# Performance work log

Hardware: AMD Instinct MI355X
Metric: run time of the kernel (lower is better)

Reference implementation:

```python
import jax, jax.numpy as jnp
import numpy as np

B, N, T = 1024, 16, 256


def setup_inputs() -> dict:
    key = jax.random.key(0)
    k1, k2, k3 = jax.random.split(key, 3)
    prediction = jax.random.normal(k1, (B, N, T), dtype=jnp.float32)
    target = jax.random.normal(k2, (B, N, T), dtype=jnp.float32)
    # cov must be symmetric positive definite per (batch, time): A A^T + I
    A = 0.3 * jax.random.normal(k3, (B, T, N, N), dtype=jnp.float32)
    cov_bt = A @ jnp.swapaxes(A, -1, -2) + jnp.eye(N, dtype=jnp.float32)  # [B,T,N,N]
    cov = jnp.transpose(cov_bt, (0, 2, 3, 1))  # [B,N,N,T] as the module expects
    return {"prediction": prediction, "target": target, "cov": cov}


def reference(prediction, target, cov):
    # prediction/target: [B,N,T], cov: [B,N,N,T]
    diff = jnp.transpose(prediction - target, (0, 2, 1))        # [B,T,N]
    cov_bt = jnp.transpose(cov, (0, 3, 1, 2))                   # [B,T,N,N]
    inv_sigma = jnp.linalg.inv(cov_bt)                          # [B,T,N,N]
    # quadratic form diff^T Sigma^{-1} diff per (batch, time)
    quad = jnp.einsum('btn,btnm,btm->bt', diff, inv_sigma, diff)  # [B,T]
    logdet = jnp.log(jnp.linalg.det(cov_bt))                      # [B,T]
    # original: sum_t [mean_b quad_t + mean_b logdet_t] / T == mean over (b,t)
    return jnp.mean(quad + logdet)
```

## Files before the change

### kernel.cpp

```cpp
#include <hip/hip_runtime.h>


#define B_ 1024
#define N_ 16
#define T_ 256
#define TRI (N_ * (N_ + 1) / 2)

__global__ __launch_bounds__(256) void gll_main(
    const float* __restrict__ pred,
    const float* __restrict__ targ,
    const float* __restrict__ cov,
    float* __restrict__ partial)
{
    const int b = blockIdx.x;
    const int t = threadIdx.x;

    float d[N_];
    const size_t pbase = (size_t)b * N_ * T_ + t;
#pragma unroll
    for (int n = 0; n < N_; ++n)
        d[n] = pred[pbase + n * T_] - targ[pbase + n * T_];

    float L[TRI];
    const size_t cbase = (size_t)b * N_ * N_ * T_ + t;
#pragma unroll
    for (int i = 0; i < N_; ++i)
#pragma unroll
        for (int j = 0; j <= i; ++j)
            L[i * (i + 1) / 2 + j] = cov[cbase + (size_t)(i * N_ + j) * T_];

    float logdet = 0.f;
#pragma unroll
    for (int i = 0; i < N_; ++i) {
#pragma unroll
        for (int j = 0; j < i; ++j) {
            float s = L[i * (i + 1) / 2 + j];
#pragma unroll
            for (int k = 0; k < j; ++k)
                s -= L[i * (i + 1) / 2 + k] * L[j * (j + 1) / 2 + k];
            L[i * (i + 1) / 2 + j] = s * L[j * (j + 1) / 2 + j];
        }
        float s = L[i * (i + 1) / 2 + i];
#pragma unroll
        for (int k = 0; k < i; ++k)
            s -= L[i * (i + 1) / 2 + k] * L[i * (i + 1) / 2 + k];
        logdet += __logf(s);
        L[i * (i + 1) / 2 + i] = rsqrtf(s);
    }

    float quad = 0.f;
#pragma unroll
    for (int i = 0; i < N_; ++i) {
        float s = d[i];
#pragma unroll
        for (int k = 0; k < i; ++k)
            s -= L[i * (i + 1) / 2 + k] * d[k];
        float y = s * L[i * (i + 1) / 2 + i];
        d[i] = y;
        quad += y * y;
    }

    float val = quad + logdet;

#pragma unroll
    for (int off = 32; off > 0; off >>= 1)
        val += __shfl_down(val, off, 64);

    __shared__ float sred[4];
    const int wave = threadIdx.x >> 6;
    const int lane = threadIdx.x & 63;
    if (lane == 0) sred[wave] = val;
    __syncthreads();
    if (threadIdx.x == 0)
        partial[b] = sred[0] + sred[1] + sred[2] + sred[3];
}

__global__ __launch_bounds__(256) void gll_reduce(
    const float* __restrict__ partial,
    float* __restrict__ out)
{
    float s = 0.f;
#pragma unroll
    for (int i = 0; i < B_ / 256; ++i)
        s += partial[threadIdx.x + i * 256];

#pragma unroll
    for (int off = 32; off > 0; off >>= 1)
        s += __shfl_down(s, off, 64);

    __shared__ float sred[4];
    const int wave = threadIdx.x >> 6;
    const int lane = threadIdx.x & 63;
    if (lane == 0) sred[wave] = s;
    __syncthreads();
    if (threadIdx.x == 0) {
        float tot = sred[0] + sred[1] + sred[2] + sred[3];
        out[0] = tot / (float)((size_t)B_ * T_);
    }
}

extern "C" void kernel_launch(void* const* d_in, const int* in_sizes, int n_in,
                              void* d_out, int out_size, void* d_ws, size_t ws_size,
                              hipStream_t stream) {
    const float* pred = (const float*)d_in[0];
    const float* targ = (const float*)d_in[1];
    const float* cov  = (const float*)d_in[2];
    float* out = (float*)d_out;
    float* partial = (float*)d_ws;

    gll_main<<<B_, 256, 0, stream>>>(pred, targ, cov, partial);
    gll_reduce<<<1, 256, 0, stream>>>(partial, out);
}
```

Measured before the change: 352.3 us.

## Split Cholesky into 8x8 blocks with Schur complement to cut register pressure

Restructures the per-thread 16x16 Cholesky into a blocked form: factor the top-left 8x8 block, solve the off-diagonal block, then factor the Schur complement of the bottom-right block. The forward solve is interleaved and loads are staged per block, so fewer values are live at once. Launch bounds now request 3 blocks per SM to raise occupancy, and loads use nontemporal hints. The blocked arithmetic does roughly the same work, but W[64] plus LA and S may still spill, and the occupancy hint could force spilling.

```diff
diff --git a/kernel.cpp b/kernel.cpp
--- a/kernel.cpp
+++ b/kernel.cpp
@@ -4,9 +4,10 @@
 #define B_ 1024
 #define N_ 16
 #define T_ 256
-#define TRI (N_ * (N_ + 1) / 2)
 
-__global__ __launch_bounds__(256) void gll_main(
+#define TIDX(i, j) ((i) * ((i) + 1) / 2 + (j))
+
+__global__ __launch_bounds__(256, 3) void gll_main(
     const float* __restrict__ pred,
     const float* __restrict__ targ,
     const float* __restrict__ cov,
@@ -15,49 +16,120 @@
     const int b = blockIdx.x;
     const int t = threadIdx.x;
 
-    float d[N_];
+    const size_t cbase = (size_t)b * N_ * N_ * T_ + t;
     const size_t pbase = (size_t)b * N_ * T_ + t;
+
+    float logdet = 0.f;
+    float quad   = 0.f;
+
+    float LA[36];
 #pragma unroll
-    for (int n = 0; n < N_; ++n)
-        d[n] = pred[pbase + n * T_] - targ[pbase + n * T_];
-
-    float L[TRI];
-    const size_t cbase = (size_t)b * N_ * N_ * T_ + t;
-#pragma unroll
-    for (int i = 0; i < N_; ++i)
+    for (int i = 0; i < 8; ++i)
 #pragma unroll
         for (int j = 0; j <= i; ++j)
-            L[i * (i + 1) / 2 + j] = cov[cbase + (size_t)(i * N_ + j) * T_];
+            LA[TIDX(i, j)] = __builtin_nontemporal_load(
+                &cov[cbase + (size_t)(i * N_ + j) * T_]);
 
-    float logdet = 0.f;
 #pragma unroll
-    for (int i = 0; i < N_; ++i) {
+    for (int i = 0; i < 8; ++i) {
 #pragma unroll
         for (int j = 0; j < i; ++j) {
-            float s = L[i * (i + 1) / 2 + j];
+            float s = LA[TIDX(i, j)];
 #pragma unroll
             for (int k = 0; k < j; ++k)
-                s -= L[i * (i + 1) / 2 + k] * L[j * (j + 1) / 2 + k];
-            L[i * (i + 1) / 2 + j] = s * L[j * (j + 1) / 2 + j];
+                s -= LA[TIDX(i, k)] * LA[TIDX(j, k)];
+            LA[TIDX(i, j)] = s * LA[TIDX(j, j)];
         }
-        float s = L[i * (i + 1) / 2 + i];
+        float s = LA[TIDX(i, i)];
 #pragma unroll
         for (int k = 0; k < i; ++k)
-            s -= L[i * (i + 1) / 2 + k] * L[i * (i + 1) / 2 + k];
+            s -= LA[TIDX(i, k)] * LA[TIDX(i, k)];
         logdet += __logf(s);
-        L[i * (i + 1) / 2 + i] = rsqrtf(s);
+        LA[TIDX(i, i)] = rsqrtf(s);
     }
 
-    float quad = 0.f;
+    float y1[8];
 #pragma unroll
-    for (int i = 0; i < N_; ++i) {
-        float s = d[i];
+    for (int i = 0; i < 8; ++i) {
+        float s = __builtin_nontemporal_load(&pred[pbase + i * T_]) -
+                  __builtin_nontemporal_load(&targ[pbase + i * T_]);
 #pragma unroll
         for (int k = 0; k < i; ++k)
-            s -= L[i * (i + 1) / 2 + k] * d[k];
-        float y = s * L[i * (i + 1) / 2 + i];
-        d[i] = y;
-        quad += y * y;
+            s -= LA[TIDX(i, k)] * y1[k];
+        y1[i] = s * LA[TIDX(i, i)];
+        quad += y1[i] * y1[i];
+    }
+
+    float W[64];
+#pragma unroll
+    for (int r = 0; r < 8; ++r)
+#pragma unroll
+        for (int j = 0; j < 8; ++j)
+            W[r * 8 + j] = __builtin_nontemporal_load(
+                &cov[cbase + (size_t)((r + 8) * N_ + j) * T_]);
+
+#pragma unroll
+    for (int r = 0; r < 8; ++r) {
+#pragma unroll
+        for (int j = 0; j < 8; ++j) {
+            float s = W[r * 8 + j];
+#pragma unroll
+            for (int k = 0; k < j; ++k)
+                s -= W[r * 8 + k] * LA[TIDX(j, k)];
+            W[r * 8 + j] = s * LA[TIDX(j, j)];
+        }
+    }
+
+    float t2[8];
+#pragma unroll
+    for (int r = 0; r < 8; ++r) {
+        float s = __builtin_nontemporal_load(&pred[pbase + (r + 8) * T_]) -
+                  __builtin_nontemporal_load(&targ[pbase + (r + 8) * T_]);
+#pragma unroll
+        for (int k = 0; k < 8; ++k)
+            s -= W[r * 8 + k] * y1[k];
+        t2[r] = s;
+    }
+
+    float S[36];
+#pragma unroll
+    for (int i = 0; i < 8; ++i)
+#pragma unroll
+        for (int j = 0; j <= i; ++j) {
+            float s = __builtin_nontemporal_load(
+                &cov[cbase + (size_t)((i + 8) * N_ + (j + 8)) * T_]);
+#pragma unroll
+            for (int k = 0; k < 8; ++k)
+                s -= W[i * 8 + k] * W[j * 8 + k];
+            S[TIDX(i, j)] = s;
+        }
+
+#pragma unroll
+    for (int i = 0; i < 8; ++i) {
+#pragma unroll
+        for (int j = 0; j < i; ++j) {
+            float s = S[TIDX(i, j)];
+#pragma unroll
+            for (int k = 0; k < j; ++k)
+                s -= S[TIDX(i, k)] * S[TIDX(j, k)];
+            S[TIDX(i, j)] = s * S[TIDX(j, j)];
+        }
+        float s = S[TIDX(i, i)];
+#pragma unroll
+        for (int k = 0; k < i; ++k)
+            s -= S[TIDX(i, k)] * S[TIDX(i, k)];
+        logdet += __logf(s);
+        S[TIDX(i, i)] = rsqrtf(s);
+    }
+
+#pragma unroll
+    for (int i = 0; i < 8; ++i) {
+        float s = t2[i];
+#pragma unroll
+        for (int k = 0; k < i; ++k)
+            s -= S[TIDX(i, k)] * t2[k];
+        t2[i] = s * S[TIDX(i, i)];
+        quad += t2[i] * t2[i];
     }
 
     float val = quad + logdet;
```

Measured after the change: 366.4 us. 4.0% more time.
